# Kernel optimization log

Hardware: AMD Instinct MI355X
Metric: run time of the kernel (lower is better)

The kernel has to match this reference:

```python
import jax, jax.numpy as jnp
import numpy as np

B, M, H, D, K, V = 32, 4096, 32, 4096, 128, 128

def setup_inputs() -> dict:
    key = jax.random.key(0)
    ks = jax.random.split(key, 7)
    s = lambda fan: 1.0 / np.sqrt(fan)
    return {
        "x": jax.random.normal(ks[0], (B, D), jnp.float32),
        "K_prev": jax.random.normal(ks[1], (B, M, K), jnp.float32),
        "V_prev": jax.random.normal(ks[2], (B, M, V), jnp.float32),
        "P_q": jax.random.normal(ks[3], (H, D, K), jnp.float32) * s(D),
        "P_k": jax.random.normal(ks[4], (D, K), jnp.float32) * s(D),
        "P_v": jax.random.normal(ks[5], (D, V), jnp.float32) * s(D),
        "P_o": jax.random.normal(ks[6], (H, D, V), jnp.float32) * s(D),
    }

def reference(x, K_prev, V_prev, P_q, P_k, P_v, P_o):
    # per-head query projection: [b,d] x [h,d,k] -> [b,h,k]
    q = jnp.einsum('bd,hdk->bhk', x, P_q)
    # shared (multi-query) K/V projection of the new token, appended to cache
    k_new = jnp.einsum('bd,dk->bk', x, P_k)          # [b,k]
    v_new = jnp.einsum('bd,dv->bv', x, P_v)          # [b,v]
    K_new = jnp.concatenate([K_prev, k_new[:, None, :]], axis=1)  # [b,m+1,k]
    V_new = jnp.concatenate([V_prev, v_new[:, None, :]], axis=1)  # [b,m+1,v]
    # attention over shared cache
    logits = jnp.einsum('bhk,bmk->bhm', q, K_new)    # [b,h,m+1]
    w = jax.nn.softmax(logits, axis=-1)
    o = jnp.einsum('bhm,bmv->bhv', w, V_new)         # [b,h,v]
    y = jnp.einsum('bhv,hdv->bd', o, P_o)            # [b,d]
    return (y, K_new, V_new)
```

## Files before the change

### kernel.cpp

```cpp
#include <hip/hip_runtime.h>

#define B_ 32
#define M_ 4096
#define M1_ 4097
#define H_ 32
#define D_ 4096

typedef float float4_ __attribute__((ext_vector_type(4)));
typedef float f32x4 __attribute__((ext_vector_type(4)));
typedef short short8 __attribute__((ext_vector_type(8)));
typedef short short4_ __attribute__((ext_vector_type(4)));

#define KOFF 131072
#define VOFF 16912384

#define Q_OFF     0u
#define O_OFF     139264u
#define YPART_OFF 270336u
#define QPART_OFF 1318912u
#define APO_OFF   1318912u
#define MSUM_OFF  2433024u

#define WAITV(n) asm volatile("s_waitcnt vmcnt(" #n ")" ::: "memory")
#define SBAR() __builtin_amdgcn_sched_barrier(0)

__device__ __forceinline__ unsigned short f2bf(float f) {
  union { float f; unsigned u; } cv; cv.f = f;
  return (unsigned short)((cv.u + 0x7FFFu + ((cv.u >> 16) & 1u)) >> 16);
}
__device__ __forceinline__ float bf2f(unsigned short b) {
  union { unsigned u; float f; } cv; cv.u = ((unsigned)b) << 16;
  return cv.f;
}
__device__ __forceinline__ short8 pack8(const float* t) {
  short8 r;
#pragma unroll
  for (int j = 0; j < 8; ++j) r[j] = (short)f2bf(t[j]);
  return r;
}
__device__ __forceinline__ short8 load8cvt(const float* __restrict__ p) {
  float t[8];
  float4_ v0 = *(const float4_*)p;
  float4_ v1 = *(const float4_*)(p + 4);
#pragma unroll
  for (int j = 0; j < 4; ++j) { t[j] = v0[j]; t[4 + j] = v1[j]; }
  return pack8(t);
}
__device__ __forceinline__ float4_ ntld4(const float* p) {
  return __builtin_nontemporal_load((const float4_*)p);
}
__device__ __forceinline__ short8 load8cvt_nt(const float* __restrict__ p) {
  float t[8];
  float4_ v0 = ntld4(p);
  float4_ v1 = ntld4(p + 4);
#pragma unroll
  for (int j = 0; j < 4; ++j) { t[j] = v0[j]; t[4 + j] = v1[j]; }
  return pack8(t);
}
__device__ __forceinline__ void load_lds16(const float* g, float* l) {
  __builtin_amdgcn_global_load_lds(
      (const __attribute__((address_space(1))) unsigned int*)g,
      (__attribute__((address_space(3))) unsigned int*)l, 16, 0, 0);
}

__global__ __launch_bounds__(256, 4) void k_proj(const float* __restrict__ x,
    const float* __restrict__ Pq, const float* __restrict__ Pk,
    const float* __restrict__ Pv, unsigned short* __restrict__ qpart)
{
  __shared__ unsigned short Wl[2][32][128];
  int bid = blockIdx.x;
  int hh = bid >> 4;
  int c  = bid & 15;
  const float* W = (hh < 32) ? (Pq + (size_t)hh * D_ * 128)
                             : ((hh == 32) ? Pk : Pv);
  int d0 = c * 256;
  int tid = threadIdx.x;
  int w = tid >> 6, l = tid & 63, l15 = l & 15, lg = l >> 4;
  int sdr = tid >> 5, sk4 = (tid & 31) * 4;
  f32x4 acc[2][2] = {};
  float4_ tmp[4];
#pragma unroll
  for (int i = 0; i < 4; ++i)
    tmp[i] = ntld4(W + (size_t)(d0 + i * 8 + sdr) * 128 + sk4);
  for (int ks = 0; ks < 8; ++ks) {
    int buf = ks & 1;
#pragma unroll
    for (int i = 0; i < 4; ++i) {
      short4_ s;
#pragma unroll
      for (int j = 0; j < 4; ++j) s[j] = (short)f2bf(tmp[i][j]);
      *(short4_*)&Wl[buf][i * 8 + sdr][sk4] = s;
    }
    if (ks < 7) {
#pragma unroll
      for (int i = 0; i < 4; ++i)
        tmp[i] = ntld4(W + (size_t)(d0 + (ks + 1) * 32 + i * 8 + sdr) * 128 + sk4);
    }
    __syncthreads();
    int dk = d0 + ks * 32 + lg * 8;
    short8 af[2];
#pragma unroll
    for (int bt = 0; bt < 2; ++bt)
      af[bt] = load8cvt(x + (size_t)(bt * 16 + l15) * D_ + dk);
    short8 bf[2];
#pragma unroll
    for (int nti = 0; nti < 2; ++nti) {
      int col = (2 * w + nti) * 16 + l15;
      short8 t;
#pragma unroll
      for (int j = 0; j < 8; ++j) t[j] = (short)Wl[buf][lg * 8 + j][col];
      bf[nti] = t;
    }
#pragma unroll
    for (int bt = 0; bt < 2; ++bt)
#pragma unroll
      for (int nti = 0; nti < 2; ++nti)
        acc[bt][nti] = __builtin_amdgcn_mfma_f32_16x16x32_bf16(af[bt], bf[nti], acc[bt][nti], 0, 0, 0);
  }
#pragma unroll
  for (int bt = 0; bt < 2; ++bt)
#pragma unroll
    for (int nti = 0; nti < 2; ++nti) {
      int k = (2 * w + nti) * 16 + l15;
#pragma unroll
      for (int i = 0; i < 4; ++i) {
        int b = bt * 16 + lg * 4 + i;
        __builtin_nontemporal_store(f2bf(acc[bt][nti][i]),
            &qpart[(size_t)((c * 34 + hh) * 32 + b) * 128 + k]);
      }
    }
}

__global__ __launch_bounds__(256) void k_reduce_q(const unsigned short* __restrict__ qpart,
    float* __restrict__ q, float* __restrict__ dout)
{
  int idx = blockIdx.x * 256 + threadIdx.x;
  if (idx >= 34 * 32 * 128) return;
  float s = 0.f;
#pragma unroll
  for (int cc = 0; cc < 16; ++cc)
    s += bf2f(__builtin_nontemporal_load(&qpart[(size_t)cc * 139264 + idx]));
  q[idx] = s;
  int hh = idx >> 12;
  if (hh >= 32) {
    int b = (idx >> 7) & 31, k = idx & 127;
    size_t off = (hh == 32) ? (size_t)KOFF : (size_t)VOFF;
    __builtin_nontemporal_store(s, &dout[off + ((size_t)b * M1_ + M_) * 128 + k]);
  }
}

#define ISSUE(T, KR, VB) do { \
  const float* Kc_ = Kb + (T) * 16 * 128; \
  const float* Vc_ = Vb + (T) * 16 * 128; \
  const float* Krow_ = Kc_ + (size_t)l15 * 128; \
  _Pragma("unroll") \
  for (int ks = 0; ks < 4; ++ks) { \
    KR[2 * ks]     = ntld4(Krow_ + ks * 32 + lg * 8); \
    KR[2 * ks + 1] = ntld4(Krow_ + ks * 32 + lg * 8 + 4); \
  } \
  _Pragma("unroll") \
  for (int i = 0; i < 8; ++i) load_lds16(Vc_ + i * 256 + l * 4, VB + i * 256); \
} while (0)

#define DO_CHUNK(T, KR, VB) do { \
   \
  float* Knrow_ = Knb + (T) * 16 * 128 + (size_t)l15 * 128; \
  _Pragma("unroll") \
  for (int ks = 0; ks < 4; ++ks) { \
    __builtin_nontemporal_store(KR[2 * ks],     (float4_*)(Knrow_ + ks * 32 + lg * 8)); \
    __builtin_nontemporal_store(KR[2 * ks + 1], (float4_*)(Knrow_ + ks * 32 + lg * 8 + 4)); \
  } \
   \
  float* Vnc_ = Vnb + (T) * 16 * 128; \
  _Pragma("unroll") \
  for (int i = 0; i < 8; ++i) { \
    float4_ t_ = *(const float4_*)(VB + (i * 64 + l) * 4); \
    __builtin_nontemporal_store(t_, (float4_*)(Vnc_ + (size_t)(i * 64 + l) * 4)); \
  } \
   \
  short8 kf_[4]; \
  _Pragma("unroll") \
  for (int ks = 0; ks < 4; ++ks) { \
    float tt_[8]; \
    _Pragma("unroll") \
    for (int j = 0; j < 4; ++j) { tt_[j] = KR[2 * ks][j]; tt_[4 + j] = KR[2 * ks + 1][j]; } \
    kf_[ks] = pack8(tt_); \
  } \
   \
  f32x4 sacc_[2] = {}; \
  _Pragma("unroll") \
  for (int ks = 0; ks < 4; ++ks) \
    _Pragma("unroll") \
    for (int ht = 0; ht < 2; ++ht) \
      sacc_[ht] = __builtin_amdgcn_mfma_f32_16x16x32_bf16(af[ht][ks], kf_[ks], sacc_[ht], 0, 0, 0); \
   \
  _Pragma("unroll") \
  for (int ht = 0; ht < 2; ++ht) { \
    f32x4 mx_; \
    _Pragma("unroll") \
    for (int i = 0; i < 4; ++i) { \
      float v_ = sacc_[ht][i]; \
      v_ = fmaxf(v_, __shfl_xor(v_, 1)); v_ = fmaxf(v_, __shfl_xor(v_, 2)); \
      v_ = fmaxf(v_, __shfl_xor(v_, 4)); v_ = fmaxf(v_, __shfl_xor(v_, 8)); \
      mx_[i] = v_; \
    } \
    f32x4 fsc_; \
    _Pragma("unroll") \
    for (int i = 0; i < 4; ++i) { \
      float mn_ = fmaxf(mrun[ht][i], mx_[i]); \
      fsc_[i] = __expf(mrun[ht][i] - mn_); \
      mrun[ht][i] = mn_; \
    } \
    _Pragma("unroll") \
    for (int vt = 0; vt < 8; ++vt) oacc[ht][vt] *= fsc_; \
    _Pragma("unroll") \
    for (int i = 0; i < 4; ++i) { \
      float p_ = __expf(sacc_[ht][i] - mrun[ht][i]); \
      lsum[ht][i] = lsum[ht][i] * fsc_[i] + p_; \
      Plds[w][ht * 16 + lg * 4 + i][l15] = f2bf(p_); \
    } \
  } \
  asm volatile("" ::: "memory"); \
   \
  short8 z_ = {}; \
  short8 pa_[2]; \
  _Pragma("unroll") \
  for (int ht = 0; ht < 2; ++ht) \
    pa_[ht] = (lg < 2) ? *(const short8*)&Plds[w][ht * 16 + l15][lg * 8] : z_; \
  _Pragma("unroll") \
  for (int vt = 0; vt < 8; ++vt) { \
    short8 bfv_ = z_; \
    if (lg < 2) { \
      float t_[8]; \
      _Pragma("unroll") \
      for (int j = 0; j < 8; ++j) t_[j] = VB[(lg * 8 + j) * 128 + vt * 16 + l15]; \
      bfv_ = pack8(t_); \
    } \
    _Pragma("unroll") \
    for (int ht = 0; ht < 2; ++ht) \
      oacc[ht][vt] = __builtin_amdgcn_mfma_f32_16x16x32_bf16(pa_[ht], bfv_, oacc[ht][vt], 0, 0, 0); \
  } \
} while (0)

__global__ __launch_bounds__(256, 2) void k_attn(const float* __restrict__ Kp,
    const float* __restrict__ Vp, const float* __restrict__ q,
    float* __restrict__ dout, unsigned short* __restrict__ apo,
    float* __restrict__ msum)
{
  __shared__ float Vbuf[4][2][2048];
  __shared__ unsigned short Plds[4][32][16];
  __shared__ float Mh[4][32], Sh[4][32];
  int bid = blockIdx.x;
  int b = bid >> 4;
  int tid = threadIdx.x, w = tid >> 6, l = tid & 63, l15 = l & 15, lg = l >> 4;
  int wid = (bid & 15) * 4 + w;
  const float* Kb = Kp + ((size_t)b * M_ + wid * 64) * 128;
  const float* Vb = Vp + ((size_t)b * M_ + wid * 64) * 128;
  float* Knb = dout + KOFF + ((size_t)b * M1_ + wid * 64) * 128;
  float* Vnb = dout + VOFF + ((size_t)b * M1_ + wid * 64) * 128;
  float* vb0 = &Vbuf[w][0][0];
  float* vb1 = &Vbuf[w][1][0];

  short8 af[2][4];
#pragma unroll
  for (int ks = 0; ks < 4; ++ks)
#pragma unroll
    for (int ht = 0; ht < 2; ++ht)
      af[ht][ks] = load8cvt(q + (size_t)((ht * 16 + l15) * 32 + b) * 128 + ks * 32 + lg * 8);

  float4_ krA[8], krB[8];
  f32x4 mrun[2], lsum[2], oacc[2][8];
#pragma unroll
  for (int ht = 0; ht < 2; ++ht) {
#pragma unroll
    for (int i = 0; i < 4; ++i) { mrun[ht][i] = -3e38f; lsum[ht][i] = 0.f; }
#pragma unroll
    for (int vt = 0; vt < 8; ++vt) oacc[ht][vt] = f32x4{0.f, 0.f, 0.f, 0.f};
  }

  ISSUE(0, krA, vb0); SBAR();
  ISSUE(1, krB, vb1); SBAR();
  WAITV(16); SBAR();
  DO_CHUNK(0, krA, vb0);
  ISSUE(2, krA, vb0); SBAR();
  WAITV(32); SBAR();
  DO_CHUNK(1, krB, vb1);
  ISSUE(3, krB, vb1); SBAR();
  WAITV(32); SBAR();
  DO_CHUNK(2, krA, vb0);
  WAITV(16); SBAR();
  DO_CHUNK(3, krB, vb1);

#pragma unroll
  for (int ht = 0; ht < 2; ++ht)
#pragma unroll
    for (int i = 0; i < 4; ++i) {
      float s = lsum[ht][i];
      s += __shfl_xor(s, 1); s += __shfl_xor(s, 2);
      s += __shfl_xor(s, 4); s += __shfl_xor(s, 8);
      lsum[ht][i] = s;
    }
  if (l15 == 0) {
#pragma unroll
    for (int ht = 0; ht < 2; ++ht)
#pragma unroll
      for (int i = 0; i < 4; ++i) {
        int h = ht * 16 + lg * 4 + i;
        Mh[w][h] = mrun[ht][i];
        Sh[w][h] = lsum[ht][i];
      }
  }
  __syncthreads();
  float* Ob = &Vbuf[w][0][0];
#pragma unroll
  for (int ht = 0; ht < 2; ++ht)
#pragma unroll
    for (int i = 0; i < 4; ++i) {
      int h = ht * 16 + lg * 4 + i;
      float ms = fmaxf(fmaxf(Mh[0][h], Mh[1][h]), fmaxf(Mh[2][h], Mh[3][h]));
      float f = __expf(mrun[ht][i] - ms);
#pragma unroll
      for (int vt = 0; vt < 8; ++vt)
        Ob[h * 128 + vt * 16 + l15] = oacc[ht][vt][i] * f;
    }
  __syncthreads();
  int blk = bid & 15;
  size_t sblk = ((size_t)b * 16 + blk) * 32;
  if (tid < 32) {
    int h = tid;
    float ms = fmaxf(fmaxf(Mh[0][h], Mh[1][h]), fmaxf(Mh[2][h], Mh[3][h]));
    float ss = Sh[0][h] * __expf(Mh[0][h] - ms) + Sh[1][h] * __expf(Mh[1][h] - ms)
             + Sh[2][h] * __expf(Mh[2][h] - ms) + Sh[3][h] * __expf(Mh[3][h] - ms);
    msum[(sblk + h) * 2]     = ms;
    msum[(sblk + h) * 2 + 1] = ss;
  }
  const float* Vall = &Vbuf[0][0][0];
  for (int idx = tid; idx < 4096; idx += 256) {
    float s = Vall[idx] + Vall[4096 + idx] + Vall[8192 + idx] + Vall[12288 + idx];
    __builtin_nontemporal_store(f2bf(s), &apo[(sblk + (idx >> 7)) * 128 + (idx & 127)]);
  }
}

__global__ __launch_bounds__(256) void k_combine(const unsigned short* __restrict__ apo,
    const float* __restrict__ msum, const float* __restrict__ q, float* __restrict__ o)
{
  __shared__ float redN[4][128];
  __shared__ float redD[4];
  int bid = blockIdx.x;
  int b = bid >> 5, h = bid & 31;
  int tid = threadIdx.x, w = tid >> 6, l = tid & 63;

  const float* qh = q + (size_t)(h * 32 + b) * 128;
  const float* kn = q + (size_t)(1024 + b) * 128;
  const float* vn = q + (size_t)(1056 + b) * 128;
  float e = qh[2 * l] * kn[2 * l] + qh[2 * l + 1] * kn[2 * l + 1];
#pragma unroll
  for (int d = 1; d < 64; d <<= 1) e += __shfl_xor(e, d);

  float gm = (l < 16) ? msum[((size_t)(b * 16 + l) * 32 + h) * 2] : -3e38f;
#pragma unroll
  for (int d = 1; d < 64; d <<= 1) gm = fmaxf(gm, __shfl_xor(gm, d));
  gm = fmaxf(gm, e);
  float pe = __expf(e - gm);

  float num0 = 0.f, num1 = 0.f, den = 0.f;
#pragma unroll
  for (int i = 0; i < 4; ++i) {
    int cc = w * 4 + i;
    size_t slot = (size_t)(b * 16 + cc) * 32 + h;
    float sc = __expf(msum[slot * 2] - gm);
    den += sc * msum[slot * 2 + 1];
    unsigned pp = __builtin_nontemporal_load((const unsigned*)&apo[slot * 128 + l * 2]);
    num0 += sc * bf2f((unsigned short)(pp & 0xFFFFu));
    num1 += sc * bf2f((unsigned short)(pp >> 16));
  }
  redN[w][l * 2] = num0;
  redN[w][l * 2 + 1] = num1;
  if (l == 0) redD[w] = den + (w == 0 ? pe : 0.f);
  __syncthreads();
  if (tid < 128) {
    float num = redN[0][tid] + redN[1][tid] + redN[2][tid] + redN[3][tid] + pe * vn[tid];
    float dd  = redD[0] + redD[1] + redD[2] + redD[3];
    o[((size_t)(b * 32 + h)) * 128 + tid] = num / dd;
  }
}

__global__ __launch_bounds__(256) void k_out(const float* __restrict__ o,
    const float* __restrict__ Po, unsigned short* __restrict__ ypart)
{
  int bid = blockIdx.x;
  int dt = bid >> 3, hg = bid & 7;
  int tid = threadIdx.x, w = tid >> 6, l = tid & 63, l15 = l & 15, lg = l >> 4;
  int d = dt * 64 + w * 16 + l15;
  f32x4 acc[2] = {};
  for (int hi = 0; hi < 4; ++hi) {
    int h = hg * 4 + hi;
#pragma unroll
    for (int ks = 0; ks < 4; ++ks) {
      short8 af[2];
#pragma unroll
      for (int bt = 0; bt < 2; ++bt)
        af[bt] = load8cvt(o + ((size_t)((bt * 16 + l15) * 32 + h)) * 128 + ks * 32 + lg * 8);
      short8 bf = load8cvt_nt(Po + ((size_t)h * D_ + d) * 128 + ks * 32 + lg * 8);
#pragma unroll
      for (int bt = 0; bt < 2; ++bt)
        acc[bt] = __builtin_amdgcn_mfma_f32_16x16x32_bf16(af[bt], bf, acc[bt], 0, 0, 0);
    }
  }
#pragma unroll
  for (int bt = 0; bt < 2; ++bt)
#pragma unroll
    for (int i = 0; i < 4; ++i) {
      int b = bt * 16 + lg * 4 + i;
      __builtin_nontemporal_store(f2bf(acc[bt][i]),
          &ypart[((size_t)(hg * 32 + b)) * 4096 + d]);
    }
}

__global__ __launch_bounds__(256) void k_reduce_y(const unsigned short* __restrict__ ypart,
    float* __restrict__ dout)
{
  int idx = blockIdx.x * 256 + threadIdx.x;
  float s = 0.f;
#pragma unroll
  for (int g = 0; g < 8; ++g)
    s += bf2f(__builtin_nontemporal_load(&ypart[(size_t)g * 131072 + idx]));
  dout[idx] = s;
}

extern "C" void kernel_launch(void* const* d_in, const int* in_sizes, int n_in,
                              void* d_out, int out_size, void* d_ws, size_t ws_size,
                              hipStream_t stream) {
  (void)in_sizes; (void)n_in; (void)out_size; (void)ws_size;
  const float* x  = (const float*)d_in[0];
  const float* Kp = (const float*)d_in[1];
  const float* Vp = (const float*)d_in[2];
  const float* Pq = (const float*)d_in[3];
  const float* Pk = (const float*)d_in[4];
  const float* Pv = (const float*)d_in[5];
  const float* Po = (const float*)d_in[6];
  float* out = (float*)d_out;
  float* ws  = (float*)d_ws;
  float* q     = ws + Q_OFF;
  float* o     = ws + O_OFF;
  unsigned short* ypart = (unsigned short*)(ws + YPART_OFF);
  unsigned short* qpart = (unsigned short*)(ws + QPART_OFF);
  unsigned short* apo   = (unsigned short*)(ws + APO_OFF);
  float* msum  = ws + MSUM_OFF;

  hipLaunchKernelGGL(k_proj,     dim3(544),  dim3(256), 0, stream, x, Pq, Pk, Pv, qpart);
  hipLaunchKernelGGL(k_reduce_q, dim3(544),  dim3(256), 0, stream, qpart, q, out);
  hipLaunchKernelGGL(k_attn,     dim3(512),  dim3(256), 0, stream, Kp, Vp, q, out, apo, msum);
  hipLaunchKernelGGL(k_combine,  dim3(1024), dim3(256), 0, stream, apo, msum, q, o);
  hipLaunchKernelGGL(k_out,      dim3(512),  dim3(256), 0, stream, o, Po, ypart);
  hipLaunchKernelGGL(k_reduce_y, dim3(512),  dim3(256), 0, stream, ypart, out);
}
```

Before: 124.6 us.

## Split cache copy into separate blocks within fused attention kernel launch

Moves the K/V cache copy-out out of the attention waves and into 4096 extra copy-only blocks in the same launch, so attention blocks only read K/V. The attention V buffer is reduced to a single buffer with a finer-grained K/V issue/wait schedule, and occupancy is raised to 4 blocks per SM. The cross-wave partial output is stored as bf16 in LDS. This reads K/V from HBM twice (once for copy, once for attention), which the L2/MALL may or may not absorb, and the single V buffer reduces overlap.

```diff
diff --git a/kernel.cpp b/kernel.cpp
--- a/kernel.cpp
+++ b/kernel.cpp
@@ -149,35 +149,22 @@
   }
 }
 
-#define ISSUE(T, KR, VB) do { \
-  const float* Kc_ = Kb + (T) * 16 * 128; \
-  const float* Vc_ = Vb + (T) * 16 * 128; \
-  const float* Krow_ = Kc_ + (size_t)l15 * 128; \
+#define ISSUE_K(T, KR) do { \
+  const float* Krow_ = Kb + (T) * 2048 + (size_t)l15 * 128; \
   _Pragma("unroll") \
   for (int ks = 0; ks < 4; ++ks) { \
-    KR[2 * ks]     = ntld4(Krow_ + ks * 32 + lg * 8); \
-    KR[2 * ks + 1] = ntld4(Krow_ + ks * 32 + lg * 8 + 4); \
+    KR[2 * ks]     = *(const float4_*)(Krow_ + ks * 32 + lg * 8); \
+    KR[2 * ks + 1] = *(const float4_*)(Krow_ + ks * 32 + lg * 8 + 4); \
   } \
+} while (0)
+
+#define ISSUE_V(T) do { \
+  const float* Vc_ = Vb + (T) * 2048; \
   _Pragma("unroll") \
   for (int i = 0; i < 8; ++i) load_lds16(Vc_ + i * 256 + l * 4, VB + i * 256); \
 } while (0)
 
-#define DO_CHUNK(T, KR, VB) do { \
-   \
-  float* Knrow_ = Knb + (T) * 16 * 128 + (size_t)l15 * 128; \
-  _Pragma("unroll") \
-  for (int ks = 0; ks < 4; ++ks) { \
-    __builtin_nontemporal_store(KR[2 * ks],     (float4_*)(Knrow_ + ks * 32 + lg * 8)); \
-    __builtin_nontemporal_store(KR[2 * ks + 1], (float4_*)(Knrow_ + ks * 32 + lg * 8 + 4)); \
-  } \
-   \
-  float* Vnc_ = Vnb + (T) * 16 * 128; \
-  _Pragma("unroll") \
-  for (int i = 0; i < 8; ++i) { \
-    float4_ t_ = *(const float4_*)(VB + (i * 64 + l) * 4); \
-    __builtin_nontemporal_store(t_, (float4_*)(Vnc_ + (size_t)(i * 64 + l) * 4)); \
-  } \
-   \
+#define CHUNK_QK(KR) do { \
   short8 kf_[4]; \
   _Pragma("unroll") \
   for (int ks = 0; ks < 4; ++ks) { \
@@ -186,14 +173,12 @@
     for (int j = 0; j < 4; ++j) { tt_[j] = KR[2 * ks][j]; tt_[4 + j] = KR[2 * ks + 1][j]; } \
     kf_[ks] = pack8(tt_); \
   } \
-   \
   f32x4 sacc_[2] = {}; \
   _Pragma("unroll") \
   for (int ks = 0; ks < 4; ++ks) \
     _Pragma("unroll") \
     for (int ht = 0; ht < 2; ++ht) \
       sacc_[ht] = __builtin_amdgcn_mfma_f32_16x16x32_bf16(af[ht][ks], kf_[ks], sacc_[ht], 0, 0, 0); \
-   \
   _Pragma("unroll") \
   for (int ht = 0; ht < 2; ++ht) { \
     f32x4 mx_; \
@@ -221,7 +206,9 @@
     } \
   } \
   asm volatile("" ::: "memory"); \
-   \
+} while (0)
+
+#define CHUNK_PV() do { \
   short8 z_ = {}; \
   short8 pa_[2]; \
   _Pragma("unroll") \
@@ -242,24 +229,43 @@
   } \
 } while (0)
 
-__global__ __launch_bounds__(256, 2) void k_attn(const float* __restrict__ Kp,
+__global__ __launch_bounds__(256, 4) void k_fused(const float* __restrict__ Kp,
     const float* __restrict__ Vp, const float* __restrict__ q,
     float* __restrict__ dout, unsigned short* __restrict__ apo,
     float* __restrict__ msum)
 {
-  __shared__ float Vbuf[4][2][2048];
+  __shared__ float Vbuf[4][2048];
   __shared__ unsigned short Plds[4][32][16];
   __shared__ float Mh[4][32], Sh[4][32];
   int bid = blockIdx.x;
+  int tid = threadIdx.x;
+
+  if (bid >= 512) {
+    int cb = bid - 512;
+    int arr = cb >> 11;
+    int blk = cb & 2047;
+    const float4_* src = (const float4_*)(arr ? Vp : Kp);
+    float* dstbase = dout + (arr ? VOFF : KOFF);
+    size_t f0 = (size_t)blk * 2048;
+    size_t b = f0 >> 17;
+    size_t r0 = f0 & 131071;
+    float* dst = dstbase + b * ((size_t)M1_ * 128);
+    float4_ t[8];
+#pragma unroll
+    for (int i = 0; i < 8; ++i) t[i] = src[f0 + i * 256 + tid];
+    SBAR();
+#pragma unroll
+    for (int i = 0; i < 8; ++i)
+      __builtin_nontemporal_store(t[i], (float4_*)(dst + (r0 + i * 256 + tid) * 4));
+    return;
+  }
+
   int b = bid >> 4;
-  int tid = threadIdx.x, w = tid >> 6, l = tid & 63, l15 = l & 15, lg = l >> 4;
+  int w = tid >> 6, l = tid & 63, l15 = l & 15, lg = l >> 4;
   int wid = (bid & 15) * 4 + w;
   const float* Kb = Kp + ((size_t)b * M_ + wid * 64) * 128;
   const float* Vb = Vp + ((size_t)b * M_ + wid * 64) * 128;
-  float* Knb = dout + KOFF + ((size_t)b * M1_ + wid * 64) * 128;
-  float* Vnb = dout + VOFF + ((size_t)b * M1_ + wid * 64) * 128;
-  float* vb0 = &Vbuf[w][0][0];
-  float* vb1 = &Vbuf[w][1][0];
+  float* VB = &Vbuf[w][0];
 
   short8 af[2][4];
 #pragma unroll
@@ -278,18 +284,30 @@
     for (int vt = 0; vt < 8; ++vt) oacc[ht][vt] = f32x4{0.f, 0.f, 0.f, 0.f};
   }
 
-  ISSUE(0, krA, vb0); SBAR();
-  ISSUE(1, krB, vb1); SBAR();
-  WAITV(16); SBAR();
-  DO_CHUNK(0, krA, vb0);
-  ISSUE(2, krA, vb0); SBAR();
-  WAITV(32); SBAR();
-  DO_CHUNK(1, krB, vb1);
-  ISSUE(3, krB, vb1); SBAR();
-  WAITV(32); SBAR();
-  DO_CHUNK(2, krA, vb0);
-  WAITV(16); SBAR();
-  DO_CHUNK(3, krB, vb1);
+  ISSUE_K(0, krA); SBAR();
+  ISSUE_V(0); SBAR();
+  WAITV(8); SBAR();
+  ISSUE_K(1, krB); SBAR();
+  CHUNK_QK(krA);
+  WAITV(8); SBAR();
+  CHUNK_PV();
+  ISSUE_V(1); SBAR();
+  WAITV(8); SBAR();
+  ISSUE_K(2, krA); SBAR();
+  CHUNK_QK(krB);
+  WAITV(8); SBAR();
+  CHUNK_PV();
+  ISSUE_V(2); SBAR();
+  WAITV(8); SBAR();
+  ISSUE_K(3, krB); SBAR();
+  CHUNK_QK(krA);
+  WAITV(8); SBAR();
+  CHUNK_PV();
+  ISSUE_V(3); SBAR();
+  WAITV(8); SBAR();
+  CHUNK_QK(krB);
+  WAITV(0); SBAR();
+  CHUNK_PV();
 
 #pragma unroll
   for (int ht = 0; ht < 2; ++ht)
@@ -311,7 +329,7 @@
       }
   }
   __syncthreads();
-  float* Ob = &Vbuf[w][0][0];
+  unsigned short* ObU = (unsigned short*)&Vbuf[w][0];
 #pragma unroll
   for (int ht = 0; ht < 2; ++ht)
 #pragma unroll
@@ -321,7 +339,7 @@
       float f = __expf(mrun[ht][i] - ms);
 #pragma unroll
       for (int vt = 0; vt < 8; ++vt)
-        Ob[h * 128 + vt * 16 + l15] = oacc[ht][vt][i] * f;
+        ObU[h * 128 + vt * 16 + l15] = f2bf(oacc[ht][vt][i] * f);
     }
   __syncthreads();
   int blk = bid & 15;
@@ -334,9 +352,9 @@
     msum[(sblk + h) * 2]     = ms;
     msum[(sblk + h) * 2 + 1] = ss;
   }
-  const float* Vall = &Vbuf[0][0][0];
+  const unsigned short* VU = (const unsigned short*)&Vbuf[0][0];
   for (int idx = tid; idx < 4096; idx += 256) {
-    float s = Vall[idx] + Vall[4096 + idx] + Vall[8192 + idx] + Vall[12288 + idx];
+    float s = bf2f(VU[idx]) + bf2f(VU[4096 + idx]) + bf2f(VU[8192 + idx]) + bf2f(VU[12288 + idx]);
     __builtin_nontemporal_store(f2bf(s), &apo[(sblk + (idx >> 7)) * 128 + (idx & 127)]);
   }
 }
@@ -450,7 +468,7 @@
 
   hipLaunchKernelGGL(k_proj,     dim3(544),  dim3(256), 0, stream, x, Pq, Pk, Pv, qpart);
   hipLaunchKernelGGL(k_reduce_q, dim3(544),  dim3(256), 0, stream, qpart, q, out);
-  hipLaunchKernelGGL(k_attn,     dim3(512),  dim3(256), 0, stream, Kp, Vp, q, out, apo, msum);
+  hipLaunchKernelGGL(k_fused,    dim3(4608), dim3(256), 0, stream, Kp, Vp, q, out, apo, msum);
   hipLaunchKernelGGL(k_combine,  dim3(1024), dim3(256), 0, stream, apo, msum, q, o);
   hipLaunchKernelGGL(k_out,      dim3(512),  dim3(256), 0, stream, o, Po, ypart);
   hipLaunchKernelGGL(k_reduce_y, dim3(512),  dim3(256), 0, stream, ypart, out);
```

Measured after the change: 174.1 us. +39.7%, slower.
